# Kernel optimization log

Measured on AMD Instinct MI355X. Metric: run time of the kernel, lower is better.

The kernel has to match this reference:

```python
import jax, jax.numpy as jnp
import numpy as np
import math

CAPACITY = 1024      # expert_capacity; >= max expert load so no tokens are dropped
NUM_HEADS = 16
ROPE_BASE = 10000.0
RMS_EPS = 1e-6


def _rmsnorm(x, w):
    rms = jnp.sqrt(jnp.mean(x * x, axis=-1, keepdims=True) + RMS_EPS)
    return x / rms * w


def _rope_tables(seq_len, head_dim):
    inv_freq = 1.0 / (ROPE_BASE ** (jnp.arange(0, head_dim, 2, dtype=jnp.float32) / head_dim))
    freqs = jnp.arange(seq_len, dtype=jnp.float32)[:, None] * inv_freq[None, :]
    emb = jnp.concatenate([freqs, freqs], axis=-1)            # [S, hd]
    return jnp.cos(emb)[None, None], jnp.sin(emb)[None, None]  # [1,1,S,hd]


def _rotate_half(x):
    h = x.shape[-1] // 2
    return jnp.concatenate([-x[..., h:], x[..., :h]], axis=-1)


def setup_inputs() -> dict:
    key = jax.random.key(0)
    ks = jax.random.split(key, 8)
    H, I, E = 1024, 4096, 8
    s = 0.02  # init scale keeps activations numerically sane
    return {
        "x": jax.random.normal(ks[0], (1, 2048, H), dtype=jnp.float32),
        "attn_norm_w": jnp.ones((H,), jnp.float32),
        "qkv_w": jax.random.normal(ks[1], (3 * H, H), jnp.float32) * s,
        "o_w": jax.random.normal(ks[2], (H, H), jnp.float32) * s,
        "ffn_norm_w": jnp.ones((H,), jnp.float32),
        "router_w": jax.random.normal(ks[3], (E, H), jnp.float32) * s,
        "wg": jax.random.normal(ks[4], (E, I, H), jnp.float32) * s,
        "wu": jax.random.normal(ks[5], (E, I, H), jnp.float32) * s,
        "wd": jax.random.normal(ks[6], (E, H, I), jnp.float32) * s,
        "position_ids": jnp.arange(2048, dtype=jnp.int64)[None, :],
    }


def _block(x, attn_norm_w, qkv_w, o_w, ffn_norm_w, router_w, wg, wu, wd):
    B, S, H = x.shape
    hd = H // NUM_HEADS
    K = 2  # num_experts_per_tok
    E = router_w.shape[0]

    # ---- attention (RoPE + causal SDPA) ----
    xn = _rmsnorm(x, attn_norm_w)
    qkv = xn @ qkv_w.T                                  # [B,S,3H]
    q, k, v = jnp.split(qkv, 3, axis=-1)
    def heads(t):
        return t.reshape(B, S, NUM_HEADS, hd).transpose(0, 2, 1, 3)  # [B,nh,S,hd]
    q, k, v = heads(q), heads(k), heads(v)
    cos, sin = _rope_tables(S, hd)
    q = q * cos + _rotate_half(q) * sin
    k = k * cos + _rotate_half(k) * sin
    scores = jnp.einsum("bhqd,bhkd->bhqk", q, k) / math.sqrt(hd)
    causal = jnp.tril(jnp.ones((S, S), bool))
    scores = jnp.where(causal[None, None], scores, -jnp.inf)
    attn = jnp.einsum("bhqk,bhkd->bhqd", jax.nn.softmax(scores, axis=-1), v)
    attn = attn.transpose(0, 2, 1, 3).reshape(B, S, H) @ o_w.T
    x = x + attn

    # ---- MoE SwiGLU FFN ----
    xn2 = _rmsnorm(x, ffn_norm_w)
    xf = xn2.reshape(-1, H)                              # [N,H]
    N = xf.shape[0]
    probs = jax.nn.softmax(xf @ router_w.T, axis=-1)     # [N,E]
    w, idx = jax.lax.top_k(probs, K)                     # [N,K]
    w = w / jnp.sum(w, axis=-1, keepdims=True)
    onehot = jax.nn.one_hot(idx, E, dtype=xf.dtype)      # [N,K,E]
    comb = onehot.sum(1)                                 # [N,E] in {0,1}
    w_ne = (w[..., None] * onehot).sum(1)                # [N,E]
    pos = jnp.cumsum(comb, axis=0) - 1.0                 # slot within expert
    valid = (comb > 0) & (pos < CAPACITY)
    pc = jnp.clip(pos, 0, CAPACITY - 1).astype(jnp.int32)  # [N,E]
    e_ids = jnp.broadcast_to(jnp.arange(E, dtype=jnp.int32)[None, :], (N, E))

    contrib = xf[:, None, :] * valid[..., None].astype(xf.dtype)  # [N,E,H]
    buf = jnp.zeros((E, CAPACITY, H), xf.dtype).at[
        e_ids.reshape(-1), pc.reshape(-1)].add(contrib.reshape(-1, H))  # [E,C,H]

    g = jnp.einsum("ech,eih->eci", buf, wg)
    u = jnp.einsum("ech,eih->eci", buf, wu)
    y = jnp.einsum("eci,ehi->ech", jax.nn.silu(g) * u, wd)  # [E,C,H]

    gathered = y[e_ids, pc]                               # [N,E,H]
    moe_out = (gathered * (w_ne * valid.astype(xf.dtype))[..., None]).sum(1)
    x = x + moe_out.reshape(B, S, H)

    aux_loss = jnp.var(comb.mean(0), ddof=1) * E          # torch.var unbiased
    return x, aux_loss


def reference(x, attn_norm_w, qkv_w, o_w, ffn_norm_w, router_w, wg, wu, wd, position_ids):
    # position_ids only enables RoPE in the original; values are not used.
    return _block(x, attn_norm_w, qkv_w, o_w, ffn_norm_w, router_w, wg, wu, wd)
```

## Files before the change

### kernel.cpp

```cpp
#include <hip/hip_runtime.h>
#include <math.h>

#define SEQ   2048
#define HID   1024
#define NHEAD 16
#define HDIM  64
#define NEXP  8
#define IDIM  4096
#define CAPE  1024
#define QKVW  3072

typedef __bf16    bf16x8 __attribute__((ext_vector_type(8)));
typedef __bf16    bf16x4 __attribute__((ext_vector_type(4)));
typedef _Float16  f16x8  __attribute__((ext_vector_type(8)));
typedef _Float16  f16x4  __attribute__((ext_vector_type(4)));
typedef float     f32x4  __attribute__((ext_vector_type(4)));

__device__ __forceinline__ void gld16(const void* g, void* l) {
  __builtin_amdgcn_global_load_lds((const __attribute__((address_space(1))) void*)g,
                                   (__attribute__((address_space(3))) void*)l, 16, 0, 0);
}

__global__ __launch_bounds__(256) void k_rmsnorm(const float* __restrict__ x,
                                                 const float* __restrict__ w,
                                                 float* __restrict__ out,
                                                 __bf16* __restrict__ out_bf,
                                                 _Float16* __restrict__ out_h,
                                                 _Float16* __restrict__ out_l) {
  const int row = blockIdx.x, t = threadIdx.x;
  float4 v = ((const float4*)(x + (size_t)row * HID))[t];
  float ss = v.x*v.x + v.y*v.y + v.z*v.z + v.w*v.w;
  #pragma unroll
  for (int off = 32; off; off >>= 1) ss += __shfl_down(ss, off);
  __shared__ float red[4];
  if ((t & 63) == 0) red[t >> 6] = ss;
  __syncthreads();
  const float inv = rsqrtf((red[0] + red[1] + red[2] + red[3]) * (1.0f / HID) + 1e-6f);
  float4 wv = ((const float4*)w)[t];
  float4 o = make_float4(v.x*inv*wv.x, v.y*inv*wv.y, v.z*inv*wv.z, v.w*inv*wv.w);
  if (out) ((float4*)(out + (size_t)row * HID))[t] = o;
  if (out_bf) {
    bf16x4 ob; ob[0] = (__bf16)o.x; ob[1] = (__bf16)o.y; ob[2] = (__bf16)o.z; ob[3] = (__bf16)o.w;
    *(bf16x4*)(out_bf + (size_t)row * HID + t * 4) = ob;
  }
  if (out_h) {
    f16x4 oh, ol;
    const float e0 = o.x, e1 = o.y, e2 = o.z, e3 = o.w;
    oh[0] = (_Float16)e0; ol[0] = (_Float16)(e0 - (float)oh[0]);
    oh[1] = (_Float16)e1; ol[1] = (_Float16)(e1 - (float)oh[1]);
    oh[2] = (_Float16)e2; ol[2] = (_Float16)(e2 - (float)oh[2]);
    oh[3] = (_Float16)e3; ol[3] = (_Float16)(e3 - (float)oh[3]);
    *(f16x4*)(out_h + (size_t)row * HID + t * 4) = oh;
    *(f16x4*)(out_l + (size_t)row * HID + t * 4) = ol;
  }
}

__global__ __launch_bounds__(256) void k_cvt_bf16(const float* __restrict__ in,
                                                  __bf16* __restrict__ out,
                                                  long n8) {
  const long i = ((long)blockIdx.x * 256 + threadIdx.x);
  if (i >= n8) return;
  const float4 a = *(const float4*)(in + i * 8);
  const float4 b = *(const float4*)(in + i * 8 + 4);
  bf16x8 o;
  o[0] = (__bf16)a.x; o[1] = (__bf16)a.y; o[2] = (__bf16)a.z; o[3] = (__bf16)a.w;
  o[4] = (__bf16)b.x; o[5] = (__bf16)b.y; o[6] = (__bf16)b.z; o[7] = (__bf16)b.w;
  *(bf16x8*)(out + i * 8) = o;
}

__global__ __launch_bounds__(256) void k_split_f16(const float* __restrict__ in,
                                                   _Float16* __restrict__ oh,
                                                   _Float16* __restrict__ ol,
                                                   long n8) {
  const long i = ((long)blockIdx.x * 256 + threadIdx.x);
  if (i >= n8) return;
  const float4 a = *(const float4*)(in + i * 8);
  const float4 b = *(const float4*)(in + i * 8 + 4);
  float e[8] = {a.x, a.y, a.z, a.w, b.x, b.y, b.z, b.w};
  f16x8 h, l;
  #pragma unroll
  for (int j = 0; j < 8; ++j) {
    h[j] = (_Float16)e[j];
    l[j] = (_Float16)(e[j] - (float)h[j]);
  }
  *(f16x8*)(oh + i * 8) = h;
  *(f16x8*)(ol + i * 8) = l;
}

__global__ __launch_bounds__(256, 2) void k_lin(const _Float16* __restrict__ Ah,
                                                const _Float16* __restrict__ Al,
                                                const _Float16* __restrict__ Bh,
                                                const _Float16* __restrict__ Bl,
                                                const float* __restrict__ res,
                                                float* __restrict__ C,
                                                int N, int Kd) {
  const int m0 = blockIdx.y * 128, n0 = blockIdx.x * 128;
  __shared__ __align__(16) _Float16 Ash[128 * 32];
  __shared__ __align__(16) _Float16 Asl[128 * 32];
  __shared__ __align__(16) _Float16 Bsh[128 * 32];
  __shared__ __align__(16) _Float16 Bsl[128 * 32];
  const int t = threadIdx.x, lane = t & 63, w = t >> 6;
  const int wr = w & 1, wc = w >> 1;
  const int sr = t >> 2, sk = (t & 3) * 8;
  const size_t a0 = (size_t)(m0 + sr) * Kd, a1 = (size_t)(m0 + 64 + sr) * Kd;
  const size_t b0 = (size_t)(n0 + sr) * Kd, b1 = (size_t)(n0 + 64 + sr) * Kd;
  f32x4 acc[4][4];
  #pragma unroll
  for (int i = 0; i < 4; ++i)
    #pragma unroll
    for (int j = 0; j < 4; ++j) acc[i][j] = (f32x4)(0.f);

  for (int kk = 0; kk < Kd; kk += 32) {
    gld16(Ah + a0 + kk + sk, Ash + w * 512);
    gld16(Ah + a1 + kk + sk, Ash + 2048 + w * 512);
    gld16(Al + a0 + kk + sk, Asl + w * 512);
    gld16(Al + a1 + kk + sk, Asl + 2048 + w * 512);
    gld16(Bh + b0 + kk + sk, Bsh + w * 512);
    gld16(Bh + b1 + kk + sk, Bsh + 2048 + w * 512);
    gld16(Bl + b0 + kk + sk, Bsl + w * 512);
    gld16(Bl + b1 + kk + sk, Bsl + 2048 + w * 512);
    __syncthreads();
    const int fo = (lane & 15) * 32 + (lane >> 4) * 8;
    f16x8 ah[4], al[4], bh[4], bl[4];
    #pragma unroll
    for (int i = 0; i < 4; ++i) {
      ah[i] = *(const f16x8*)&Ash[(wr * 64 + i * 16) * 32 + fo];
      al[i] = *(const f16x8*)&Asl[(wr * 64 + i * 16) * 32 + fo];
      bh[i] = *(const f16x8*)&Bsh[(wc * 64 + i * 16) * 32 + fo];
      bl[i] = *(const f16x8*)&Bsl[(wc * 64 + i * 16) * 32 + fo];
    }
    #pragma unroll
    for (int i = 0; i < 4; ++i)
      #pragma unroll
      for (int j = 0; j < 4; ++j) {
        acc[i][j] = __builtin_amdgcn_mfma_f32_16x16x32_f16(al[i], bh[j], acc[i][j], 0, 0, 0);
        acc[i][j] = __builtin_amdgcn_mfma_f32_16x16x32_f16(ah[i], bl[j], acc[i][j], 0, 0, 0);
        acc[i][j] = __builtin_amdgcn_mfma_f32_16x16x32_f16(ah[i], bh[j], acc[i][j], 0, 0, 0);
      }
    __syncthreads();
  }
  const int cb = lane & 15, rb = (lane >> 4) * 4;
  #pragma unroll
  for (int i = 0; i < 4; ++i)
    #pragma unroll
    for (int r = 0; r < 4; ++r) {
      const int rr = m0 + wr * 64 + i * 16 + rb + r;
      #pragma unroll
      for (int j = 0; j < 4; ++j) {
        const int cc = n0 + wc * 64 + j * 16 + cb;
        float v = acc[i][j][r];
// ... 70 lines not shown
    f16x8 vh0, vl0, vh1, vl1;
    #pragma unroll
    for (int j = 0; j < 8; ++j) {
      const float v = vt[sc + j][d];
      vh0[j] = (_Float16)v; vl0[j] = (_Float16)(v - (float)vh0[j]);
    }
    #pragma unroll
    for (int j = 0; j < 8; ++j) {
      const float v = vt[sc + 8 + j][d];
      vh1[j] = (_Float16)v; vl1[j] = (_Float16)(v - (float)vh1[j]);
    }
    const size_t vo = ((size_t)h * HDIM + d) * SEQ + s0 + sc;
    *(f16x8*)(Vth + vo) = vh0; *(f16x8*)(Vth + vo + 8) = vh1;
    *(f16x8*)(Vtl + vo) = vl0; *(f16x8*)(Vtl + vo + 8) = vl1;
  }
}

__global__ __launch_bounds__(256) void k_attn2(
    const _Float16* __restrict__ Qh, const _Float16* __restrict__ Ql,
    const _Float16* __restrict__ Kh, const _Float16* __restrict__ Kl,
    const _Float16* __restrict__ Vth, const _Float16* __restrict__ Vtl,
    _Float16* __restrict__ attn_h, _Float16* __restrict__ attn_l) {
  const int h = blockIdx.x;
  const int qt = (int)gridDim.y - 1 - (int)blockIdx.y;
  const int t = threadIdx.x, lane = t & 63, w = t >> 6;
  const int m_ = lane & 15, quad = lane >> 4;

  __shared__ __align__(16) _Float16 Ksh[2][64][32];
  __shared__ __align__(16) _Float16 Ksl[2][64][32];
  __shared__ __align__(16) _Float16 Vsh[4][64][16];
  __shared__ __align__(16) _Float16 Vsl[4][64][16];
  __shared__ __align__(16) _Float16 Ph[4][16][72];
  __shared__ __align__(16) _Float16 Pl[4][16][72];

  const int q0 = qt * 64 + w * 16;
  const _Float16* qbh = Qh + ((size_t)h * SEQ + q0 + m_) * 64 + quad * 8;
  const _Float16* qbl = Ql + ((size_t)h * SEQ + q0 + m_) * 64 + quad * 8;
  const f16x8 qh0 = *(const f16x8*)(qbh);
  const f16x8 qh1 = *(const f16x8*)(qbh + 32);
  const f16x8 ql0 = *(const f16x8*)(qbl);
  const f16x8 ql1 = *(const f16x8*)(qbl + 32);

  f32x4 o[4];
  #pragma unroll
  for (int nt = 0; nt < 4; ++nt) o[nt] = (f32x4)(0.f);
  float m_r[4] = {-1e30f, -1e30f, -1e30f, -1e30f};
  float l_r[4] = {0.f, 0.f, 0.f, 0.f};

  for (int kt = 0; kt <= qt; ++kt) {
    if (w == 0) {
      #pragma unroll
      for (int c = 0; c < 2; ++c)
        #pragma unroll
        for (int kb = 0; kb < 4; ++kb)
          gld16(Kh + ((size_t)h * SEQ + kt * 64 + kb * 16 + (lane >> 2)) * 64 + c * 32 + (lane & 3) * 8,
                &Ksh[c][kb * 16][0]);
    } else if (w == 1) {
      #pragma unroll
      for (int c = 0; c < 2; ++c)
        #pragma unroll
        for (int kb = 0; kb < 4; ++kb)
          gld16(Kl + ((size_t)h * SEQ + kt * 64 + kb * 16 + (lane >> 2)) * 64 + c * 32 + (lane & 3) * 8,
                &Ksl[c][kb * 16][0]);
    } else if (w == 2) {
      #pragma unroll
      for (int g = 0; g < 4; ++g)
        #pragma unroll
        for (int hd = 0; hd < 2; ++hd)
          gld16(Vth + ((size_t)h * HDIM + hd * 32 + (lane >> 1)) * SEQ + kt * 64 + g * 16 + (lane & 1) * 8,
                &Vsh[g][hd * 32][0]);
    } else {
      #pragma unroll
      for (int g = 0; g < 4; ++g)
        #pragma unroll
        for (int hd = 0; hd < 2; ++hd)
          gld16(Vtl + ((size_t)h * HDIM + hd * 32 + (lane >> 1)) * SEQ + kt * 64 + g * 16 + (lane & 1) * 8,
                &Vsl[g][hd * 32][0]);
    }
    __syncthreads();

    f32x4 s4[4];
    #pragma unroll
    for (int nt = 0; nt < 4; ++nt) s4[nt] = (f32x4)(0.f);
    #pragma unroll
    for (int c = 0; c < 2; ++c) {
      const f16x8 qhc = c ? qh1 : qh0;
      const f16x8 qlc = c ? ql1 : ql0;
      #pragma unroll
      for (int nt = 0; nt < 4; ++nt) {
        const f16x8 kh8 = *(const f16x8*)&Ksh[c][nt * 16 + m_][quad * 8];
        const f16x8 kl8 = *(const f16x8*)&Ksl[c][nt * 16 + m_][quad * 8];
        s4[nt] = __builtin_amdgcn_mfma_f32_16x16x32_f16(qlc, kh8, s4[nt], 0, 0, 0);
        s4[nt] = __builtin_amdgcn_mfma_f32_16x16x32_f16(qhc, kl8, s4[nt], 0, 0, 0);
        s4[nt] = __builtin_amdgcn_mfma_f32_16x16x32_f16(qhc, kh8, s4[nt], 0, 0, 0);
      }
    }
    if (kt == qt) {
      #pragma unroll
      for (int nt = 0; nt < 4; ++nt)
        #pragma unroll
        for (int r = 0; r < 4; ++r)
          if (nt * 16 + m_ > w * 16 + quad * 4 + r) s4[nt][r] = -1e30f;
    }
    float mx[4];
    #pragma unroll
    for (int r = 0; r < 4; ++r)
      mx[r] = fmaxf(fmaxf(s4[0][r], s4[1][r]), fmaxf(s4[2][r], s4[3][r]));
    #pragma unroll
    for (int msk = 1; msk < 16; msk <<= 1)
      #pragma unroll
      for (int r = 0; r < 4; ++r) mx[r] = fmaxf(mx[r], __shfl_xor(mx[r], msk));
    float al[4];
    #pragma unroll
    for (int r = 0; r < 4; ++r) {
      const float mn = fmaxf(m_r[r], mx[r]);
      al[r] = expf(m_r[r] - mn);
      m_r[r] = mn;
    }
    float rs[4] = {0.f, 0.f, 0.f, 0.f};
    #pragma unroll
    for (int nt = 0; nt < 4; ++nt) {
      #pragma unroll
      for (int r = 0; r < 4; ++r) {
        const float p = expf(s4[nt][r] - m_r[r]);
        rs[r] += p;
        const _Float16 ph = (_Float16)p;
        Ph[w][quad * 4 + r][nt * 16 + m_] = ph;
        Pl[w][quad * 4 + r][nt * 16 + m_] = (_Float16)(p - (float)ph);
      }
    }
    #pragma unroll
    for (int msk = 1; msk < 16; msk <<= 1)
      #pragma unroll
      for (int r = 0; r < 4; ++r) rs[r] += __shfl_xor(rs[r], msk);
    #pragma unroll
    for (int r = 0; r < 4; ++r) l_r[r] = l_r[r] * al[r] + rs[r];
    #pragma unroll
    for (int nt = 0; nt < 4; ++nt)
      #pragma unroll
      for (int r = 0; r < 4; ++r) o[nt][r] *= al[r];

    #pragma unroll
    for (int c = 0; c < 2; ++c) {
      const f16x8 pah = *(const f16x8*)&Ph[w][m_][c * 32 + quad * 8];
      const f16x8 pal = *(const f16x8*)&Pl[w][m_][c * 32 + quad * 8];
      #pragma unroll
      for (int nt = 0; nt < 4; ++nt) {
        const f16x8 vh8 = *(const f16x8*)&Vsh[c * 2 + (quad >> 1)][nt * 16 + m_][(quad & 1) * 8];
        const f16x8 vl8 = *(const f16x8*)&Vsl[c * 2 + (quad >> 1)][nt * 16 + m_][(quad & 1) * 8];
        o[nt] = __builtin_amdgcn_mfma_f32_16x16x32_f16(pal, vh8, o[nt], 0, 0, 0);
        o[nt] = __builtin_amdgcn_mfma_f32_16x16x32_f16(pah, vl8, o[nt], 0, 0, 0);
        o[nt] = __builtin_amdgcn_mfma_f32_16x16x32_f16(pah, vh8, o[nt], 0, 0, 0);
      }
    }
    __syncthreads();
  }

  float inv[4];
  #pragma unroll
  for (int r = 0; r < 4; ++r) inv[r] = 1.0f / l_r[r];
  #pragma unroll
  for (int nt = 0; nt < 4; ++nt)
    #pragma unroll
    for (int r = 0; r < 4; ++r) {
      const float v = o[nt][r] * inv[r];
      const _Float16 hi = (_Float16)v;
      const size_t idx = ((size_t)(q0 + quad * 4 + r)) * HID + h * HDIM + nt * 16 + m_;
      attn_h[idx] = hi;
      attn_l[idx] = (_Float16)(v - (float)hi);
    }
}

__global__ __launch_bounds__(64) void k_router(const float* __restrict__ xn2,
                                               const float* __restrict__ rw,
                                               int* __restrict__ tidx,
                                               float* __restrict__ tw) {
  const int n = blockIdx.x, lane = threadIdx.x;
  float lg[8] = {0.f,0.f,0.f,0.f,0.f,0.f,0.f,0.f};
  #pragma unroll
  for (int i = 0; i < 4; ++i) {
    float4 xv = ((const float4*)(xn2 + (size_t)n * HID))[lane + 64 * i];
    #pragma unroll
    for (int e = 0; e < 8; ++e) {
      float4 wv = ((const float4*)(rw + (size_t)e * HID))[lane + 64 * i];
      lg[e] += xv.x*wv.x + xv.y*wv.y + xv.z*wv.z + xv.w*wv.w;
    }
  }
  #pragma unroll
  for (int e = 0; e < 8; ++e) {
    #pragma unroll
    for (int off = 32; off; off >>= 1) lg[e] += __shfl_xor(lg[e], off);
  }
  if (lane == 0) {
    int e1 = 0; float l1 = lg[0];
    #pragma unroll
    for (int e = 1; e < 8; ++e) if (lg[e] > l1) { l1 = lg[e]; e1 = e; }
    int e2 = -1; float l2 = -INFINITY;
    #pragma unroll
    for (int e = 0; e < 8; ++e) if (e != e1 && lg[e] > l2) { l2 = lg[e]; e2 = e; }
    const float w1 = 1.0f / (1.0f + expf(l2 - l1));
    tidx[n * 2] = e1; tidx[n * 2 + 1] = e2;
    tw[n * 2] = w1;  tw[n * 2 + 1] = 1.0f - w1;
  }
}

__global__ __launch_bounds__(512) void k_scan(const int* __restrict__ tidx,
                                              int* __restrict__ slotk,
                                              int* __restrict__ perm,
                                              int* __restrict__ counts,
                                              float* __restrict__ aux_out) {
  const int t = threadIdx.x;
  const int e = t >> 6, lane = t & 63;
  __shared__ int cls[8];
  int offset = 0;
  for (int chunk = 0; chunk < SEQ / 64; ++chunk) {
    const int n = chunk * 64 + lane;
    const int i0 = tidx[n * 2], i1 = tidx[n * 2 + 1];
    const bool bit = (i0 == e) || (i1 == e);
    const unsigned long long mask = __ballot(bit);
    const int pos = offset + __popcll(mask & ((1ull << lane) - 1ull));
    if (bit) {
      const int kk = (i0 == e) ? 0 : 1;
      slotk[n * 2 + kk] = pos;
      if (pos < CAPE) perm[e * CAPE + pos] = n;
    }
    offset += __popcll(mask);
  }
  if (lane == 0) { counts[e] = offset; cls[e] = offset; }
  __syncthreads();
  if (t == 0) {
    float mean = 0.f;
    for (int i = 0; i < 8; ++i) mean += (float)cls[i];
    mean /= (8.0f * (float)SEQ);
    float var = 0.f;
    for (int i = 0; i < 8; ++i) {
      const float f = (float)cls[i] / (float)SEQ;
      var += (f - mean) * (f - mean);
    }
    var /= 7.0f;
    aux_out[0] = var * 8.0f;
  }
}

__global__ __launch_bounds__(256, 2) void k_moe_gu(const __bf16* __restrict__ X,
                                                   const __bf16* __restrict__ Wg,
                                                   const __bf16* __restrict__ Wu,
                                                   const int* __restrict__ perm,
                                                   const int* __restrict__ counts,
                                                   __bf16* __restrict__ act) {
  const int e = blockIdx.z;
  const int rows = min(counts[e], CAPE);
  const int m0 = blockIdx.y * 128;
  if (m0 >= rows) return;
  const int n0 = blockIdx.x * 128;
  __shared__ __align__(16) __bf16 As[128 * 32];
  __shared__ __align__(16) __bf16 Bgs[128 * 32];
  __shared__ __align__(16) __bf16 Bus[128 * 32];
  const int t = threadIdx.x;
  const int lane = t & 63, w = t >> 6;
  const int wr = w & 1, wc = w >> 1;
  const int sr = t >> 2;
  const int sk = (t & 3) * 8;
  const int gr0 = m0 + sr, gr1 = m0 + 64 + sr;
  const size_t arow0 = (size_t)((gr0 < rows) ? perm[e * CAPE + gr0] : 0) * HID;
  const size_t arow1 = (size_t)((gr1 < rows) ? perm[e * CAPE + gr1] : 0) * HID;
  const __bf16* gB = Wg + (size_t)e * IDIM * HID;
  const __bf16* uB = Wu + (size_t)e * IDIM * HID;
  const size_t brow0 = (size_t)(n0 + sr) * HID, brow1 = (size_t)(n0 + 64 + sr) * HID;
  f32x4 accg[4][4], accu[4][4];
  #pragma unroll
  for (int i = 0; i < 4; ++i)
    #pragma unroll
    for (int j = 0; j < 4; ++j) { accg[i][j] = (f32x4)(0.f); accu[i][j] = (f32x4)(0.f); }

  for (int kk = 0; kk < HID; kk += 32) {
    gld16(X + arow0 + kk + sk, As + w * 512);
    gld16(X + arow1 + kk + sk, As + 2048 + w * 512);
    gld16(gB + brow0 + kk + sk, Bgs + w * 512);
    gld16(gB + brow1 + kk + sk, Bgs + 2048 + w * 512);
    gld16(uB + brow0 + kk + sk, Bus + w * 512);
    gld16(uB + brow1 + kk + sk, Bus + 2048 + w * 512);
    __syncthreads();
    bf16x8 a[4], bg[4], bu[4];
    #pragma unroll
    for (int i = 0; i < 4; ++i) {
      const int fo = (lane & 15) * 32 + (lane >> 4) * 8;
      a[i]  = *(const bf16x8*)&As[(wr * 64 + i * 16) * 32 + fo];
      bg[i] = *(const bf16x8*)&Bgs[(wc * 64 + i * 16) * 32 + fo];
      bu[i] = *(const bf16x8*)&Bus[(wc * 64 + i * 16) * 32 + fo];
    }
    #pragma unroll
    for (int i = 0; i < 4; ++i)
      #pragma unroll
      for (int j = 0; j < 4; ++j) {
        accg[i][j] = __builtin_amdgcn_mfma_f32_16x16x32_bf16(a[i], bg[j], accg[i][j], 0, 0, 0);
        accu[i][j] = __builtin_amdgcn_mfma_f32_16x16x32_bf16(a[i], bu[j], accu[i][j], 0, 0, 0);
      }
    __syncthreads();
  }
  const int cb = lane & 15, rb = (lane >> 4) * 4;
  #pragma unroll
  for (int i = 0; i < 4; ++i)
    #pragma unroll
    for (int r = 0; r < 4; ++r) {
      const int rr = m0 + wr * 64 + i * 16 + rb + r;
      if (rr < rows) {
        #pragma unroll
        for (int j = 0; j < 4; ++j) {
          const float g = accg[i][j][r], u = accu[i][j][r];
          const float v = g / (1.f + expf(-g)) * u;
          act[((size_t)e * CAPE + rr) * IDIM + n0 + wc * 64 + j * 16 + cb] = (__bf16)v;
        }
      }
    }
}

__global__ __launch_bounds__(256, 2) void k_moe_down(const __bf16* __restrict__ act,
                                                     const __bf16* __restrict__ Wd,
                                                     const int* __restrict__ counts,
                                                     float* __restrict__ y) {
  const int e = blockIdx.z;
  const int rows = min(counts[e], CAPE);
  const int m0 = blockIdx.y * 128;
  if (m0 >= rows) return;
  const int n0 = blockIdx.x * 128;
  __shared__ __align__(16) __bf16 As[128 * 32];
  __shared__ __align__(16) __bf16 Bs[128 * 32];
  const int t = threadIdx.x;
  const int lane = t & 63, w = t >> 6;
  const int wr = w & 1, wc = w >> 1;
  const int sr = t >> 2;
  const int sk = (t & 3) * 8;
  const __bf16* Ab = act + ((size_t)e * CAPE) * IDIM;
  const __bf16* Bb = Wd + (size_t)e * HID * IDIM;
  const size_t arow0 = (size_t)(m0 + sr) * IDIM, arow1 = (size_t)(m0 + 64 + sr) * IDIM;
  const size_t brow0 = (size_t)(n0 + sr) * IDIM, brow1 = (size_t)(n0 + 64 + sr) * IDIM;
  f32x4 acc[4][4];
  #pragma unroll
  for (int i = 0; i < 4; ++i)
    #pragma unroll
    for (int j = 0; j < 4; ++j) acc[i][j] = (f32x4)(0.f);

  for (int kk = 0; kk < IDIM; kk += 32) {
    gld16(Ab + arow0 + kk + sk, As + w * 512);
    gld16(Ab + arow1 + kk + sk, As + 2048 + w * 512);
    gld16(Bb + brow0 + kk + sk, Bs + w * 512);
    gld16(Bb + brow1 + kk + sk, Bs + 2048 + w * 512);
    __syncthreads();
    bf16x8 a[4], b[4];
    #pragma unroll
    for (int i = 0; i < 4; ++i) {
      const int fo = (lane & 15) * 32 + (lane >> 4) * 8;
      a[i] = *(const bf16x8*)&As[(wr * 64 + i * 16) * 32 + fo];
      b[i] = *(const bf16x8*)&Bs[(wc * 64 + i * 16) * 32 + fo];
    }
    #pragma unroll
    for (int i = 0; i < 4; ++i)
      #pragma unroll
      for (int j = 0; j < 4; ++j)
        acc[i][j] = __builtin_amdgcn_mfma_f32_16x16x32_bf16(a[i], b[j], acc[i][j], 0, 0, 0);
    __syncthreads();
  }
  const int cb = lane & 15, rb = (lane >> 4) * 4;
  #pragma unroll
  for (int i = 0; i < 4; ++i)
    #pragma unroll
    for (int r = 0; r < 4; ++r) {
      const int rr = m0 + wr * 64 + i * 16 + rb + r;
      if (rr < rows) {
        #pragma unroll
        for (int j = 0; j < 4; ++j)
          y[((size_t)e * CAPE + rr) * HID + n0 + wc * 64 + j * 16 + cb] = acc[i][j][r];
      }
    }
}

__global__ __launch_bounds__(256) void k_combine(const float* __restrict__ x1,
                                                 const float* __restrict__ y,
                                                 const int* __restrict__ tidx,
                                                 const float* __restrict__ tw,
                                                 const int* __restrict__ slotk,
                                                 float* __restrict__ out) {
  const int n = blockIdx.x, t = threadIdx.x;
  float4 acc = ((const float4*)(x1 + (size_t)n * HID))[t];
  #pragma unroll
  for (int k = 0; k < 2; ++k) {
    const int slot = slotk[n * 2 + k];
    if (slot < CAPE) {
      const int e = tidx[n * 2 + k];
      const float w = tw[n * 2 + k];
      float4 v = ((const float4*)(y + ((size_t)e * CAPE + slot) * HID))[t];
      acc.x += w * v.x; acc.y += w * v.y; acc.z += w * v.z; acc.w += w * v.w;
    }
  }
  ((float4*)(out + (size_t)n * HID))[t] = acc;
}

extern "C" void kernel_launch(void* const* d_in, const int* in_sizes, int n_in,
                              void* d_out, int out_size, void* d_ws, size_t ws_size,
                              hipStream_t stream) {
  const float* x     = (const float*)d_in[0];
  const float* anw   = (const float*)d_in[1];
  const float* qkv_w = (const float*)d_in[2];
  const float* o_w   = (const float*)d_in[3];
  const float* fnw   = (const float*)d_in[4];
  const float* rw    = (const float*)d_in[5];
  const float* wg    = (const float*)d_in[6];
  const float* wu    = (const float*)d_in[7];
  const float* wd    = (const float*)d_in[8];
  (void)in_sizes; (void)n_in; (void)out_size; (void)ws_size;
  float* out = (float*)d_out;

  float* ws = (float*)d_ws;
  size_t off = 0;
  float* qkv  = ws + off; off += (size_t)SEQ * QKVW;
  float* x1   = ws + off; off += (size_t)SEQ * HID;
  float* xn2  = ws + off; off += (size_t)SEQ * HID;
  float* ybuf = ws + off; off += (size_t)NEXP * CAPE * HID;
  float* tw   = ws + off; off += SEQ * 2;
  int* tidx   = (int*)(ws + off); off += SEQ * 2;
  int* slotk  = (int*)(ws + off); off += SEQ * 2;
  int* perm   = (int*)(ws + off); off += NEXP * CAPE;
  int* counts = (int*)(ws + off); off += 16;
  __bf16* bfbase = (__bf16*)(ws + off);
  size_t boff = 0;
  __bf16* xn2_bf = bfbase + boff; boff += (size_t)SEQ * HID;
  __bf16* wg_bf  = bfbase + boff; boff += (size_t)NEXP * IDIM * HID;
  __bf16* wu_bf  = bfbase + boff; boff += (size_t)NEXP * IDIM * HID;
  __bf16* wd_bf  = bfbase + boff; boff += (size_t)NEXP * HID * IDIM;
  __bf16* act_bf = bfbase + boff; boff += (size_t)NEXP * CAPE * IDIM;
  _Float16* f16base = (_Float16*)(bfbase + boff);
  size_t foff = 0;
  _Float16* xn_h   = f16base + foff; foff += (size_t)SEQ * HID;
  _Float16* xn_l   = f16base + foff; foff += (size_t)SEQ * HID;
  _Float16* qkvw_h = f16base + foff; foff += (size_t)QKVW * HID;
  _Float16* qkvw_l = f16base + foff; foff += (size_t)QKVW * HID;
  _Float16* attn_h = f16base + foff; foff += (size_t)SEQ * HID;
  _Float16* attn_l = f16base + foff; foff += (size_t)SEQ * HID;
  _Float16* ow_h   = f16base + foff; foff += (size_t)HID * HID;
  _Float16* ow_l   = f16base + foff; foff += (size_t)HID * HID;
  _Float16* Qhb    = f16base + foff; foff += (size_t)NHEAD * SEQ * HDIM;
  _Float16* Qlb    = f16base + foff; foff += (size_t)NHEAD * SEQ * HDIM;
  _Float16* Khb    = f16base + foff; foff += (size_t)NHEAD * SEQ * HDIM;
  _Float16* Klb    = f16base + foff; foff += (size_t)NHEAD * SEQ * HDIM;
  _Float16* Vthb   = f16base + foff; foff += (size_t)NHEAD * SEQ * HDIM;
  _Float16* Vtlb   = f16base + foff; foff += (size_t)NHEAD * SEQ * HDIM;

  const long nw8 = (long)NEXP * IDIM * HID / 8;
  const int cvtGrid = (int)((nw8 + 255) / 256);
  k_cvt_bf16<<<cvtGrid, 256, 0, stream>>>(wg, wg_bf, nw8);
  k_cvt_bf16<<<cvtGrid, 256, 0, stream>>>(wu, wu_bf, nw8);
  k_cvt_bf16<<<cvtGrid, 256, 0, stream>>>(wd, wd_bf, nw8);
  k_split_f16<<<(QKVW * HID / 8 + 255) / 256, 256, 0, stream>>>(qkv_w, qkvw_h, qkvw_l, QKVW * HID / 8);
  k_split_f16<<<(HID * HID / 8 + 255) / 256, 256, 0, stream>>>(o_w, ow_h, ow_l, HID * HID / 8);

  k_rmsnorm<<<SEQ, 256, 0, stream>>>(x, anw, nullptr, nullptr, xn_h, xn_l);
  k_lin<<<dim3(QKVW / 128, SEQ / 128), 256, 0, stream>>>(xn_h, xn_l, qkvw_h, qkvw_l, nullptr, qkv, QKVW, HID);
  k_prep<<<dim3(NHEAD, SEQ / 64), 256, 0, stream>>>(qkv, Qhb, Qlb, Khb, Klb, Vthb, Vtlb);
  k_attn2<<<dim3(NHEAD, SEQ / 64), 256, 0, stream>>>(Qhb, Qlb, Khb, Klb, Vthb, Vtlb, attn_h, attn_l);
  k_lin<<<dim3(HID / 128, SEQ / 128), 256, 0, stream>>>(attn_h, attn_l, ow_h, ow_l, x, x1, HID, HID);
  k_rmsnorm<<<SEQ, 256, 0, stream>>>(x1, fnw, xn2, xn2_bf, nullptr, nullptr);
  k_router<<<SEQ, 64, 0, stream>>>(xn2, rw, tidx, tw);
  k_scan<<<1, 512, 0, stream>>>(tidx, slotk, perm, counts, out + (size_t)SEQ * HID);
  k_moe_gu<<<dim3(IDIM / 128, CAPE / 128, NEXP), 256, 0, stream>>>(xn2_bf, wg_bf, wu_bf, perm, counts, act_bf);
  k_moe_down<<<dim3(HID / 128, CAPE / 128, NEXP), 256, 0, stream>>>(act_bf, wd_bf, counts, ybuf);
  k_combine<<<SEQ, 256, 0, stream>>>(x1, ybuf, tidx, tw, slotk, out);
}
```

Baseline: 872.8 us.

## Fuse fp32-to-bf16 weight conversion into MoE GEMMs with double-buffered loads

Drops the three standalone weight-conversion kernels. The MoE gate/up and down GEMMs now read fp32 expert weights directly, convert them to bf16 in registers, and store them into double-buffered LDS tiles, prefetching the next K tile during the MFMAs. This removes a full read and write pass over roughly 400 MB of weights. In exchange, fp32 weight data is re-read once per row tile of each expert, up to 8 times, and LDS use and register pressure rise. It also wraps the attention MFMA sections in s_setprio.

```diff
diff --git a/kernel.cpp b/kernel.cpp
--- a/kernel.cpp
+++ b/kernel.cpp
@@ -19,6 +19,13 @@
 __device__ __forceinline__ void gld16(const void* g, void* l) {
   __builtin_amdgcn_global_load_lds((const __attribute__((address_space(1))) void*)g,
                                    (__attribute__((address_space(3))) void*)l, 16, 0, 0);
+}
+
+__device__ __forceinline__ bf16x8 cvt_bf8(const float4 a, const float4 b) {
+  bf16x8 o;
+  o[0] = (__bf16)a.x; o[1] = (__bf16)a.y; o[2] = (__bf16)a.z; o[3] = (__bf16)a.w;
+  o[4] = (__bf16)b.x; o[5] = (__bf16)b.y; o[6] = (__bf16)b.z; o[7] = (__bf16)b.w;
+  return o;
 }
 
 __global__ __launch_bounds__(256) void k_rmsnorm(const float* __restrict__ x,
@@ -53,19 +60,6 @@
     *(f16x4*)(out_h + (size_t)row * HID + t * 4) = oh;
     *(f16x4*)(out_l + (size_t)row * HID + t * 4) = ol;
   }
-}
-
-__global__ __launch_bounds__(256) void k_cvt_bf16(const float* __restrict__ in,
-                                                  __bf16* __restrict__ out,
-                                                  long n8) {
-  const long i = ((long)blockIdx.x * 256 + threadIdx.x);
-  if (i >= n8) return;
-  const float4 a = *(const float4*)(in + i * 8);
-  const float4 b = *(const float4*)(in + i * 8 + 4);
-  bf16x8 o;
-  o[0] = (__bf16)a.x; o[1] = (__bf16)a.y; o[2] = (__bf16)a.z; o[3] = (__bf16)a.w;
-  o[4] = (__bf16)b.x; o[5] = (__bf16)b.y; o[6] = (__bf16)b.z; o[7] = (__bf16)b.w;
-  *(bf16x8*)(out + i * 8) = o;
 }
 
 __global__ __launch_bounds__(256) void k_split_f16(const float* __restrict__ in,
@@ -302,6 +296,7 @@
     f32x4 s4[4];
     #pragma unroll
     for (int nt = 0; nt < 4; ++nt) s4[nt] = (f32x4)(0.f);
+    __builtin_amdgcn_s_setprio(1);
     #pragma unroll
     for (int c = 0; c < 2; ++c) {
       const f16x8 qhc = c ? qh1 : qh0;
@@ -315,6 +310,7 @@
         s4[nt] = __builtin_amdgcn_mfma_f32_16x16x32_f16(qhc, kh8, s4[nt], 0, 0, 0);
       }
     }
+    __builtin_amdgcn_s_setprio(0);
     if (kt == qt) {
       #pragma unroll
       for (int nt = 0; nt < 4; ++nt)
@@ -360,6 +356,7 @@
       #pragma unroll
       for (int r = 0; r < 4; ++r) o[nt][r] *= al[r];
 
+    __builtin_amdgcn_s_setprio(1);
     #pragma unroll
     for (int c = 0; c < 2; ++c) {
       const f16x8 pah = *(const f16x8*)&Ph[w][m_][c * 32 + quad * 8];
@@ -373,6 +370,7 @@
         o[nt] = __builtin_amdgcn_mfma_f32_16x16x32_f16(pah, vh8, o[nt], 0, 0, 0);
       }
     }
+    __builtin_amdgcn_s_setprio(0);
     __syncthreads();
   }
 
@@ -463,8 +461,8 @@
 }
 
 __global__ __launch_bounds__(256, 2) void k_moe_gu(const __bf16* __restrict__ X,
-                                                   const __bf16* __restrict__ Wg,
-                                                   const __bf16* __restrict__ Wu,
+                                                   const float* __restrict__ Wg,
+                                                   const float* __restrict__ Wu,
                                                    const int* __restrict__ perm,
                                                    const int* __restrict__ counts,
                                                    __bf16* __restrict__ act) {
@@ -473,9 +471,9 @@
   const int m0 = blockIdx.y * 128;
   if (m0 >= rows) return;
   const int n0 = blockIdx.x * 128;
-  __shared__ __align__(16) __bf16 As[128 * 32];
-  __shared__ __align__(16) __bf16 Bgs[128 * 32];
-  __shared__ __align__(16) __bf16 Bus[128 * 32];
+  __shared__ __align__(16) __bf16 As[2][128 * 32];
+  __shared__ __align__(16) __bf16 Bgs[2][128 * 32];
+  __shared__ __align__(16) __bf16 Bus[2][128 * 32];
   const int t = threadIdx.x;
   const int lane = t & 63, w = t >> 6;
   const int wr = w & 1, wc = w >> 1;
@@ -484,30 +482,60 @@
   const int gr0 = m0 + sr, gr1 = m0 + 64 + sr;
   const size_t arow0 = (size_t)((gr0 < rows) ? perm[e * CAPE + gr0] : 0) * HID;
   const size_t arow1 = (size_t)((gr1 < rows) ? perm[e * CAPE + gr1] : 0) * HID;
-  const __bf16* gB = Wg + (size_t)e * IDIM * HID;
-  const __bf16* uB = Wu + (size_t)e * IDIM * HID;
-  const size_t brow0 = (size_t)(n0 + sr) * HID, brow1 = (size_t)(n0 + 64 + sr) * HID;
+  const float* gB = Wg + (size_t)e * IDIM * HID;
+  const float* uB = Wu + (size_t)e * IDIM * HID;
+  const size_t brow0 = (size_t)(n0 + sr) * HID + sk;
+  const size_t brow1 = (size_t)(n0 + 64 + sr) * HID + sk;
+  const int wb  = sr * 32 + sk;
+  const int wb2 = (64 + sr) * 32 + sk;
   f32x4 accg[4][4], accu[4][4];
   #pragma unroll
   for (int i = 0; i < 4; ++i)
     #pragma unroll
     for (int j = 0; j < 4; ++j) { accg[i][j] = (f32x4)(0.f); accu[i][j] = (f32x4)(0.f); }
 
+  {
+    gld16(X + arow0 + sk, &As[0][w * 512]);
+    gld16(X + arow1 + sk, &As[0][2048 + w * 512]);
+    const float4 g0 = *(const float4*)(gB + brow0);
+    const float4 g1 = *(const float4*)(gB + brow0 + 4);
+    const float4 g2 = *(const float4*)(gB + brow1);
+    const float4 g3 = *(const float4*)(gB + brow1 + 4);
+    const float4 u0 = *(const float4*)(uB + brow0);
+    const float4 u1 = *(const float4*)(uB + brow0 + 4);
+    const float4 u2 = *(const float4*)(uB + brow1);
+    const float4 u3 = *(const float4*)(uB + brow1 + 4);
+    *(bf16x8*)&Bgs[0][wb]  = cvt_bf8(g0, g1);
+    *(bf16x8*)&Bgs[0][wb2] = cvt_bf8(g2, g3);
+    *(bf16x8*)&Bus[0][wb]  = cvt_bf8(u0, u1);
+    *(bf16x8*)&Bus[0][wb2] = cvt_bf8(u2, u3);
+  }
+  __syncthreads();
+
+  int cur = 0;
   for (int kk = 0; kk < HID; kk += 32) {
-    gld16(X + arow0 + kk + sk, As + w * 512);
-    gld16(X + arow1 + kk + sk, As + 2048 + w * 512);
-    gld16(gB + brow0 + kk + sk, Bgs + w * 512);
-    gld16(gB + brow1 + kk + sk, Bgs + 2048 + w * 512);
-    gld16(uB + brow0 + kk + sk, Bus + w * 512);
-    gld16(uB + brow1 + kk + sk, Bus + 2048 + w * 512);
-    __syncthreads();
+    const int nxt = cur ^ 1;
+    const bool pf = (kk + 32) < HID;
+    float4 g0, g1, g2, g3, u0, u1, u2, u3;
+    if (pf) {
+      gld16(X + arow0 + kk + 32 + sk, &As[nxt][w * 512]);
+      gld16(X + arow1 + kk + 32 + sk, &As[nxt][2048 + w * 512]);
+      g0 = *(const float4*)(gB + brow0 + kk + 32);
+      g1 = *(const float4*)(gB + brow0 + kk + 36);
+      g2 = *(const float4*)(gB + brow1 + kk + 32);
+      g3 = *(const float4*)(gB + brow1 + kk + 36);
+      u0 = *(const float4*)(uB + brow0 + kk + 32);
+      u1 = *(const float4*)(uB + brow0 + kk + 36);
+      u2 = *(const float4*)(uB + brow1 + kk + 32);
+      u3 = *(const float4*)(uB + brow1 + kk + 36);
+    }
+    const int fo = (lane & 15) * 32 + (lane >> 4) * 8;
     bf16x8 a[4], bg[4], bu[4];
     #pragma unroll
     for (int i = 0; i < 4; ++i) {
-      const int fo = (lane & 15) * 32 + (lane >> 4) * 8;
-      a[i]  = *(const bf16x8*)&As[(wr * 64 + i * 16) * 32 + fo];
-      bg[i] = *(const bf16x8*)&Bgs[(wc * 64 + i * 16) * 32 + fo];
-      bu[i] = *(const bf16x8*)&Bus[(wc * 64 + i * 16) * 32 + fo];
+      a[i]  = *(const bf16x8*)&As[cur][(wr * 64 + i * 16) * 32 + fo];
+      bg[i] = *(const bf16x8*)&Bgs[cur][(wc * 64 + i * 16) * 32 + fo];
+      bu[i] = *(const bf16x8*)&Bus[cur][(wc * 64 + i * 16) * 32 + fo];
     }
     #pragma unroll
     for (int i = 0; i < 4; ++i)
@@ -516,7 +544,14 @@
         accg[i][j] = __builtin_amdgcn_mfma_f32_16x16x32_bf16(a[i], bg[j], accg[i][j], 0, 0, 0);
         accu[i][j] = __builtin_amdgcn_mfma_f32_16x16x32_bf16(a[i], bu[j], accu[i][j], 0, 0, 0);
       }
+    if (pf) {
+      *(bf16x8*)&Bgs[nxt][wb]  = cvt_bf8(g0, g1);
+      *(bf16x8*)&Bgs[nxt][wb2] = cvt_bf8(g2, g3);
+      *(bf16x8*)&Bus[nxt][wb]  = cvt_bf8(u0, u1);
+      *(bf16x8*)&Bus[nxt][wb2] = cvt_bf8(u2, u3);
+    }
     __syncthreads();
+    cur = nxt;
   }
   const int cb = lane & 15, rb = (lane >> 4) * 4;
   #pragma unroll
@@ -536,7 +571,7 @@
 }
 
 __global__ __launch_bounds__(256, 2) void k_moe_down(const __bf16* __restrict__ act,
-                                                     const __bf16* __restrict__ Wd,
+                                                     const float* __restrict__ Wd,
                                                      const int* __restrict__ counts,
                                                      float* __restrict__ y) {
   const int e = blockIdx.z;
@@ -544,42 +579,68 @@
   const int m0 = blockIdx.y * 128;
   if (m0 >= rows) return;
   const int n0 = blockIdx.x * 128;
-  __shared__ __align__(16) __bf16 As[128 * 32];
-  __shared__ __align__(16) __bf16 Bs[128 * 32];
+  __shared__ __align__(16) __bf16 As[2][128 * 32];
+  __shared__ __align__(16) __bf16 Bs[2][128 * 32];
   const int t = threadIdx.x;
   const int lane = t & 63, w = t >> 6;
   const int wr = w & 1, wc = w >> 1;
   const int sr = t >> 2;
   const int sk = (t & 3) * 8;
   const __bf16* Ab = act + ((size_t)e * CAPE) * IDIM;
-  const __bf16* Bb = Wd + (size_t)e * HID * IDIM;
-  const size_t arow0 = (size_t)(m0 + sr) * IDIM, arow1 = (size_t)(m0 + 64 + sr) * IDIM;
-  const size_t brow0 = (size_t)(n0 + sr) * IDIM, brow1 = (size_t)(n0 + 64 + sr) * IDIM;
+  const float* Bb = Wd + (size_t)e * HID * IDIM;
+  const size_t arow0 = (size_t)(m0 + sr) * IDIM + sk, arow1 = (size_t)(m0 + 64 + sr) * IDIM + sk;
+  const size_t brow0 = (size_t)(n0 + sr) * IDIM + sk, brow1 = (size_t)(n0 + 64 + sr) * IDIM + sk;
+  const int wb  = sr * 32 + sk;
+  const int wb2 = (64 + sr) * 32 + sk;
   f32x4 acc[4][4];
   #pragma unroll
   for (int i = 0; i < 4; ++i)
     #pragma unroll
     for (int j = 0; j < 4; ++j) acc[i][j] = (f32x4)(0.f);
 
+  {
+    gld16(Ab + arow0, &As[0][w * 512]);
+    gld16(Ab + arow1, &As[0][2048 + w * 512]);
+    const float4 b0 = *(const float4*)(Bb + brow0);
+    const float4 b1 = *(const float4*)(Bb + brow0 + 4);
+    const float4 b2 = *(const float4*)(Bb + brow1);
+    const float4 b3 = *(const float4*)(Bb + brow1 + 4);
+    *(bf16x8*)&Bs[0][wb]  = cvt_bf8(b0, b1);
+    *(bf16x8*)&Bs[0][wb2] = cvt_bf8(b2, b3);
+  }
+  __syncthreads();
+
+  int cur = 0;
   for (int kk = 0; kk < IDIM; kk += 32) {
-    gld16(Ab + arow0 + kk + sk, As + w * 512);
-    gld16(Ab + arow1 + kk + sk, As + 2048 + w * 512);
-    gld16(Bb + brow0 + kk + sk, Bs + w * 512);
-    gld16(Bb + brow1 + kk + sk, Bs + 2048 + w * 512);
-    __syncthreads();
+    const int nxt = cur ^ 1;
+    const bool pf = (kk + 32) < IDIM;
+    float4 b0, b1, b2, b3;
+    if (pf) {
+      gld16(Ab + arow0 + kk + 32, &As[nxt][w * 512]);
+      gld16(Ab + arow1 + kk + 32, &As[nxt][2048 + w * 512]);
+      b0 = *(const float4*)(Bb + brow0 + kk + 32);
+      b1 = *(const float4*)(Bb + brow0 + kk + 36);
+      b2 = *(const float4*)(Bb + brow1 + kk + 32);
+      b3 = *(const float4*)(Bb + brow1 + kk + 36);
+    }
+    const int fo = (lane & 15) * 32 + (lane >> 4) * 8;
     bf16x8 a[4], b[4];
     #pragma unroll
     for (int i = 0; i < 4; ++i) {
-      const int fo = (lane & 15) * 32 + (lane >> 4) * 8;
-      a[i] = *(const bf16x8*)&As[(wr * 64 + i * 16) * 32 + fo];
-      b[i] = *(const bf16x8*)&Bs[(wc * 64 + i * 16) * 32 + fo];
+      a[i] = *(const bf16x8*)&As[cur][(wr * 64 + i * 16) * 32 + fo];
+      b[i] = *(const bf16x8*)&Bs[cur][(wc * 64 + i * 16) * 32 + fo];
     }
     #pragma unroll
     for (int i = 0; i < 4; ++i)
       #pragma unroll
       for (int j = 0; j < 4; ++j)
         acc[i][j] = __builtin_amdgcn_mfma_f32_16x16x32_bf16(a[i], b[j], acc[i][j], 0, 0, 0);
+    if (pf) {
+      *(bf16x8*)&Bs[nxt][wb]  = cvt_bf8(b0, b1);
+      *(bf16x8*)&Bs[nxt][wb2] = cvt_bf8(b2, b3);
+    }
     __syncthreads();
+    cur = nxt;
   }
   const int cb = lane & 15, rb = (lane >> 4) * 4;
   #pragma unroll
@@ -645,9 +706,6 @@
   __bf16* bfbase = (__bf16*)(ws + off);
   size_t boff = 0;
   __bf16* xn2_bf = bfbase + boff; boff += (size_t)SEQ * HID;
-  __bf16* wg_bf  = bfbase + boff; boff += (size_t)NEXP * IDIM * HID;
-  __bf16* wu_bf  = bfbase + boff; boff += (size_t)NEXP * IDIM * HID;
-  __bf16* wd_bf  = bfbase + boff; boff += (size_t)NEXP * HID * IDIM;
   __bf16* act_bf = bfbase + boff; boff += (size_t)NEXP * CAPE * IDIM;
   _Float16* f16base = (_Float16*)(bfbase + boff);
   size_t foff = 0;
@@ -666,11 +724,6 @@
   _Float16* Vthb   = f16base + foff; foff += (size_t)NHEAD * SEQ * HDIM;
   _Float16* Vtlb   = f16base + foff; foff += (size_t)NHEAD * SEQ * HDIM;
 
-  const long nw8 = (long)NEXP * IDIM * HID / 8;
-  const int cvtGrid = (int)((nw8 + 255) / 256);
-  k_cvt_bf16<<<cvtGrid, 256, 0, stream>>>(wg, wg_bf, nw8);
-  k_cvt_bf16<<<cvtGrid, 256, 0, stream>>>(wu, wu_bf, nw8);
-  k_cvt_bf16<<<cvtGrid, 256, 0, stream>>>(wd, wd_bf, nw8);
   k_split_f16<<<(QKVW * HID / 8 + 255) / 256, 256, 0, stream>>>(qkv_w, qkvw_h, qkvw_l, QKVW * HID / 8);
   k_split_f16<<<(HID * HID / 8 + 255) / 256, 256, 0, stream>>>(o_w, ow_h, ow_l, HID * HID / 8);
 
@@ -682,7 +735,7 @@
   k_rmsnorm<<<SEQ, 256, 0, stream>>>(x1, fnw, xn2, xn2_bf, nullptr, nullptr);
   k_router<<<SEQ, 64, 0, stream>>>(xn2, rw, tidx, tw);
   k_scan<<<1, 512, 0, stream>>>(tidx, slotk, perm, counts, out + (size_t)SEQ * HID);
-  k_moe_gu<<<dim3(IDIM / 128, CAPE / 128, NEXP), 256, 0, stream>>>(xn2_bf, wg_bf, wu_bf, perm, counts, act_bf);
-  k_moe_down<<<dim3(HID / 128, CAPE / 128, NEXP), 256, 0, stream>>>(act_bf, wd_bf, counts, ybuf);
+  k_moe_gu<<<dim3(IDIM / 128, CAPE / 128, NEXP), 256, 0, stream>>>(xn2_bf, wg, wu, perm, counts, act_bf);
+  k_moe_down<<<dim3(HID / 128, CAPE / 128, NEXP), 256, 0, stream>>>(act_bf, wd, counts, ybuf);
   k_combine<<<SEQ, 256, 0, stream>>>(x1, ybuf, tidx, tw, slotk, out);
 }
```

New measurement: 879.4 us. No clear change (+0.8%).

## Fuse fp32-to-bf16 expert weight conversion into MoE GEMM loads; add MFMA setprio

Applied to the files above, without the earlier changes.

Drops the three standalone bf16 conversion passes over the expert weights. The MoE gate/up and down GEMMs now stage fp32 weight tiles in shared memory with an XOR swizzle and convert to bf16 in registers just before the MFMA. This removes a full read and write of about 100M weights per call, but each GEMM block now loads twice as many bytes of weights and uses more LDS, which could lower occupancy. The attention kernel also raises wave priority around its MFMA sections.

```diff
diff --git a/kernel.cpp b/kernel.cpp
--- a/kernel.cpp
+++ b/kernel.cpp
@@ -19,6 +19,13 @@
 __device__ __forceinline__ void gld16(const void* g, void* l) {
   __builtin_amdgcn_global_load_lds((const __attribute__((address_space(1))) void*)g,
                                    (__attribute__((address_space(3))) void*)l, 16, 0, 0);
+}
+
+__device__ __forceinline__ bf16x8 cvt_bf8(const float4 a, const float4 b) {
+  bf16x8 o;
+  o[0] = (__bf16)a.x; o[1] = (__bf16)a.y; o[2] = (__bf16)a.z; o[3] = (__bf16)a.w;
+  o[4] = (__bf16)b.x; o[5] = (__bf16)b.y; o[6] = (__bf16)b.z; o[7] = (__bf16)b.w;
+  return o;
 }
 
 __global__ __launch_bounds__(256) void k_rmsnorm(const float* __restrict__ x,
@@ -53,19 +60,6 @@
     *(f16x4*)(out_h + (size_t)row * HID + t * 4) = oh;
     *(f16x4*)(out_l + (size_t)row * HID + t * 4) = ol;
   }
-}
-
-__global__ __launch_bounds__(256) void k_cvt_bf16(const float* __restrict__ in,
-                                                  __bf16* __restrict__ out,
-                                                  long n8) {
-  const long i = ((long)blockIdx.x * 256 + threadIdx.x);
-  if (i >= n8) return;
-  const float4 a = *(const float4*)(in + i * 8);
-  const float4 b = *(const float4*)(in + i * 8 + 4);
-  bf16x8 o;
-  o[0] = (__bf16)a.x; o[1] = (__bf16)a.y; o[2] = (__bf16)a.z; o[3] = (__bf16)a.w;
-  o[4] = (__bf16)b.x; o[5] = (__bf16)b.y; o[6] = (__bf16)b.z; o[7] = (__bf16)b.w;
-  *(bf16x8*)(out + i * 8) = o;
 }
 
 __global__ __launch_bounds__(256) void k_split_f16(const float* __restrict__ in,
@@ -302,6 +296,7 @@
     f32x4 s4[4];
     #pragma unroll
     for (int nt = 0; nt < 4; ++nt) s4[nt] = (f32x4)(0.f);
+    __builtin_amdgcn_s_setprio(1);
     #pragma unroll
     for (int c = 0; c < 2; ++c) {
       const f16x8 qhc = c ? qh1 : qh0;
@@ -315,6 +310,7 @@
         s4[nt] = __builtin_amdgcn_mfma_f32_16x16x32_f16(qhc, kh8, s4[nt], 0, 0, 0);
       }
     }
+    __builtin_amdgcn_s_setprio(0);
     if (kt == qt) {
       #pragma unroll
       for (int nt = 0; nt < 4; ++nt)
@@ -360,6 +356,7 @@
       #pragma unroll
       for (int r = 0; r < 4; ++r) o[nt][r] *= al[r];
 
+    __builtin_amdgcn_s_setprio(1);
     #pragma unroll
     for (int c = 0; c < 2; ++c) {
       const f16x8 pah = *(const f16x8*)&Ph[w][m_][c * 32 + quad * 8];
@@ -373,6 +370,7 @@
         o[nt] = __builtin_amdgcn_mfma_f32_16x16x32_f16(pah, vh8, o[nt], 0, 0, 0);
       }
     }
+    __builtin_amdgcn_s_setprio(0);
     __syncthreads();
   }
 
@@ -463,8 +461,8 @@
 }
 
 __global__ __launch_bounds__(256, 2) void k_moe_gu(const __bf16* __restrict__ X,
-                                                   const __bf16* __restrict__ Wg,
-                                                   const __bf16* __restrict__ Wu,
+                                                   const float* __restrict__ Wg,
+                                                   const float* __restrict__ Wu,
                                                    const int* __restrict__ perm,
                                                    const int* __restrict__ counts,
                                                    __bf16* __restrict__ act) {
@@ -474,19 +472,20 @@
   if (m0 >= rows) return;
   const int n0 = blockIdx.x * 128;
   __shared__ __align__(16) __bf16 As[128 * 32];
-  __shared__ __align__(16) __bf16 Bgs[128 * 32];
-  __shared__ __align__(16) __bf16 Bus[128 * 32];
+  __shared__ __align__(16) float  Bgf[128 * 32];
+  __shared__ __align__(16) float  Buf[128 * 32];
   const int t = threadIdx.x;
   const int lane = t & 63, w = t >> 6;
   const int wr = w & 1, wc = w >> 1;
-  const int sr = t >> 2;
-  const int sk = (t & 3) * 8;
+  const int sr = t >> 2, sk = (t & 3) * 8;
   const int gr0 = m0 + sr, gr1 = m0 + 64 + sr;
   const size_t arow0 = (size_t)((gr0 < rows) ? perm[e * CAPE + gr0] : 0) * HID;
   const size_t arow1 = (size_t)((gr1 < rows) ? perm[e * CAPE + gr1] : 0) * HID;
-  const __bf16* gB = Wg + (size_t)e * IDIM * HID;
-  const __bf16* uB = Wu + (size_t)e * IDIM * HID;
-  const size_t brow0 = (size_t)(n0 + sr) * HID, brow1 = (size_t)(n0 + 64 + sr) * HID;
+  const float* gB = Wg + (size_t)e * IDIM * HID;
+  const float* uB = Wu + (size_t)e * IDIM * HID;
+  const int brow = t >> 3;
+  const int scol = ((t ^ (t >> 3)) & 7) * 4;
+  const size_t bsrc = (size_t)(n0 + brow) * HID + scol;
   f32x4 accg[4][4], accu[4][4];
   #pragma unroll
   for (int i = 0; i < 4; ++i)
@@ -496,18 +495,27 @@
   for (int kk = 0; kk < HID; kk += 32) {
     gld16(X + arow0 + kk + sk, As + w * 512);
     gld16(X + arow1 + kk + sk, As + 2048 + w * 512);
-    gld16(gB + brow0 + kk + sk, Bgs + w * 512);
-    gld16(gB + brow1 + kk + sk, Bgs + 2048 + w * 512);
-    gld16(uB + brow0 + kk + sk, Bus + w * 512);
-    gld16(uB + brow1 + kk + sk, Bus + 2048 + w * 512);
-    __syncthreads();
+    #pragma unroll
+    for (int p = 0; p < 4; ++p) {
+      gld16(gB + bsrc + (size_t)p * 32 * HID + kk, Bgf + p * 1024 + w * 256);
+      gld16(uB + bsrc + (size_t)p * 32 * HID + kk, Buf + p * 1024 + w * 256);
+    }
+    __syncthreads();
+    const int fo = (lane & 15) * 32 + (lane >> 4) * 8;
+    const int q2 = (lane >> 4) * 2;
+    const int rx = lane & 7;
+    const int p0 = ((q2) ^ rx) * 4, p1 = ((q2 | 1) ^ rx) * 4;
     bf16x8 a[4], bg[4], bu[4];
     #pragma unroll
     for (int i = 0; i < 4; ++i) {
-      const int fo = (lane & 15) * 32 + (lane >> 4) * 8;
       a[i]  = *(const bf16x8*)&As[(wr * 64 + i * 16) * 32 + fo];
-      bg[i] = *(const bf16x8*)&Bgs[(wc * 64 + i * 16) * 32 + fo];
-      bu[i] = *(const bf16x8*)&Bus[(wc * 64 + i * 16) * 32 + fo];
+      const int R = (wc * 64 + i * 16 + (lane & 15)) * 32;
+      const float4 g0 = *(const float4*)&Bgf[R + p0];
+      const float4 g1 = *(const float4*)&Bgf[R + p1];
+      const float4 u0 = *(const float4*)&Buf[R + p0];
+      const float4 u1 = *(const float4*)&Buf[R + p1];
+      bg[i] = cvt_bf8(g0, g1);
+      bu[i] = cvt_bf8(u0, u1);
     }
     #pragma unroll
     for (int i = 0; i < 4; ++i)
@@ -536,7 +544,7 @@
 }
 
 __global__ __launch_bounds__(256, 2) void k_moe_down(const __bf16* __restrict__ act,
-                                                     const __bf16* __restrict__ Wd,
+                                                     const float* __restrict__ Wd,
                                                      const int* __restrict__ counts,
                                                      float* __restrict__ y) {
   const int e = blockIdx.z;
@@ -545,16 +553,18 @@
   if (m0 >= rows) return;
   const int n0 = blockIdx.x * 128;
   __shared__ __align__(16) __bf16 As[128 * 32];
-  __shared__ __align__(16) __bf16 Bs[128 * 32];
+  __shared__ __align__(16) float  Bf[128 * 32];
   const int t = threadIdx.x;
   const int lane = t & 63, w = t >> 6;
   const int wr = w & 1, wc = w >> 1;
   const int sr = t >> 2;
   const int sk = (t & 3) * 8;
   const __bf16* Ab = act + ((size_t)e * CAPE) * IDIM;
-  const __bf16* Bb = Wd + (size_t)e * HID * IDIM;
+  const float* Bb = Wd + (size_t)e * HID * IDIM;
   const size_t arow0 = (size_t)(m0 + sr) * IDIM, arow1 = (size_t)(m0 + 64 + sr) * IDIM;
-  const size_t brow0 = (size_t)(n0 + sr) * IDIM, brow1 = (size_t)(n0 + 64 + sr) * IDIM;
+  const int brow = t >> 3;
+  const int scol = ((t ^ (t >> 3)) & 7) * 4;
+  const size_t bsrc = (size_t)(n0 + brow) * IDIM + scol;
   f32x4 acc[4][4];
   #pragma unroll
   for (int i = 0; i < 4; ++i)
@@ -564,15 +574,22 @@
   for (int kk = 0; kk < IDIM; kk += 32) {
     gld16(Ab + arow0 + kk + sk, As + w * 512);
     gld16(Ab + arow1 + kk + sk, As + 2048 + w * 512);
-    gld16(Bb + brow0 + kk + sk, Bs + w * 512);
-    gld16(Bb + brow1 + kk + sk, Bs + 2048 + w * 512);
-    __syncthreads();
+    #pragma unroll
+    for (int p = 0; p < 4; ++p)
+      gld16(Bb + bsrc + (size_t)p * 32 * IDIM + kk, Bf + p * 1024 + w * 256);
+    __syncthreads();
+    const int fo = (lane & 15) * 32 + (lane >> 4) * 8;
+    const int q2 = (lane >> 4) * 2;
+    const int rx = lane & 7;
+    const int p0 = ((q2) ^ rx) * 4, p1 = ((q2 | 1) ^ rx) * 4;
     bf16x8 a[4], b[4];
     #pragma unroll
     for (int i = 0; i < 4; ++i) {
-      const int fo = (lane & 15) * 32 + (lane >> 4) * 8;
       a[i] = *(const bf16x8*)&As[(wr * 64 + i * 16) * 32 + fo];
-      b[i] = *(const bf16x8*)&Bs[(wc * 64 + i * 16) * 32 + fo];
+      const int R = (wc * 64 + i * 16 + (lane & 15)) * 32;
+      const float4 b0 = *(const float4*)&Bf[R + p0];
+      const float4 b1 = *(const float4*)&Bf[R + p1];
+      b[i] = cvt_bf8(b0, b1);
     }
     #pragma unroll
     for (int i = 0; i < 4; ++i)
@@ -645,9 +662,6 @@
   __bf16* bfbase = (__bf16*)(ws + off);
   size_t boff = 0;
   __bf16* xn2_bf = bfbase + boff; boff += (size_t)SEQ * HID;
-  __bf16* wg_bf  = bfbase + boff; boff += (size_t)NEXP * IDIM * HID;
-  __bf16* wu_bf  = bfbase + boff; boff += (size_t)NEXP * IDIM * HID;
-  __bf16* wd_bf  = bfbase + boff; boff += (size_t)NEXP * HID * IDIM;
   __bf16* act_bf = bfbase + boff; boff += (size_t)NEXP * CAPE * IDIM;
   _Float16* f16base = (_Float16*)(bfbase + boff);
   size_t foff = 0;
@@ -666,11 +680,6 @@
   _Float16* Vthb   = f16base + foff; foff += (size_t)NHEAD * SEQ * HDIM;
   _Float16* Vtlb   = f16base + foff; foff += (size_t)NHEAD * SEQ * HDIM;
 
-  const long nw8 = (long)NEXP * IDIM * HID / 8;
-  const int cvtGrid = (int)((nw8 + 255) / 256);
-  k_cvt_bf16<<<cvtGrid, 256, 0, stream>>>(wg, wg_bf, nw8);
-  k_cvt_bf16<<<cvtGrid, 256, 0, stream>>>(wu, wu_bf, nw8);
-  k_cvt_bf16<<<cvtGrid, 256, 0, stream>>>(wd, wd_bf, nw8);
   k_split_f16<<<(QKVW * HID / 8 + 255) / 256, 256, 0, stream>>>(qkv_w, qkvw_h, qkvw_l, QKVW * HID / 8);
   k_split_f16<<<(HID * HID / 8 + 255) / 256, 256, 0, stream>>>(o_w, ow_h, ow_l, HID * HID / 8);
 
@@ -682,7 +691,7 @@
   k_rmsnorm<<<SEQ, 256, 0, stream>>>(x1, fnw, xn2, xn2_bf, nullptr, nullptr);
   k_router<<<SEQ, 64, 0, stream>>>(xn2, rw, tidx, tw);
   k_scan<<<1, 512, 0, stream>>>(tidx, slotk, perm, counts, out + (size_t)SEQ * HID);
-  k_moe_gu<<<dim3(IDIM / 128, CAPE / 128, NEXP), 256, 0, stream>>>(xn2_bf, wg_bf, wu_bf, perm, counts, act_bf);
-  k_moe_down<<<dim3(HID / 128, CAPE / 128, NEXP), 256, 0, stream>>>(act_bf, wd_bf, counts, ybuf);
+  k_moe_gu<<<dim3(IDIM / 128, CAPE / 128, NEXP), 256, 0, stream>>>(xn2_bf, wg, wu, perm, counts, act_bf);
+  k_moe_down<<<dim3(HID / 128, CAPE / 128, NEXP), 256, 0, stream>>>(act_bf, wd, counts, ybuf);
   k_combine<<<SEQ, 256, 0, stream>>>(x1, ybuf, tidx, tw, slotk, out);
 }
```

Result: faster. 830.7 us (-4.8%).
